# Kernel tuning notes

Measured on AMD Instinct MI355X. Metric: run time of the kernel, lower is better.

Reference implementation:

```python
import jax, jax.numpy as jnp
import numpy as np

NUM_BATCH, NUM_OBJ, NUM_DBOX, NUM_CLASSES = 64, 50, 8732, 2
JACCARD_THRESH = 0.5
NEGPOS_RATIO = 3
VARIANCE = (0.1, 0.2)


def setup_inputs() -> dict:
    key = jax.random.key(0)
    k1, k2, k3, k4, k5, k6 = jax.random.split(key, 6)
    loc_data = jax.random.normal(k1, (NUM_BATCH, NUM_DBOX, 4), dtype=jnp.float32)
    conf_data = jax.random.normal(k2, (NUM_BATCH, NUM_DBOX, NUM_CLASSES), dtype=jnp.float32)
    # default boxes in center-size form (cx, cy, w, h)
    cxcy = jax.random.uniform(k3, (NUM_DBOX, 2), minval=0.05, maxval=0.95)
    wh = jax.random.uniform(k4, (NUM_DBOX, 2), minval=0.05, maxval=0.4)
    dbox_list = jnp.concatenate([cxcy, wh], axis=1).astype(jnp.float32)
    # ground-truth boxes in point form [xmin,ymin,xmax,ymax] plus label (class 0 -> conf label 1)
    tc = jax.random.uniform(k5, (NUM_BATCH, NUM_OBJ, 2), minval=0.15, maxval=0.85)
    twh = jax.random.uniform(k6, (NUM_BATCH, NUM_OBJ, 2), minval=0.05, maxval=0.3)
    truths = jnp.concatenate([tc - twh / 2, tc + twh / 2], axis=-1)
    labels = jnp.zeros((NUM_BATCH, NUM_OBJ, 1), dtype=jnp.float32)
    targets = jnp.concatenate([truths, labels], axis=-1).astype(jnp.float32)
    return {"loc_data": loc_data, "conf_data": conf_data, "dbox_list": dbox_list, "targets": targets}


def point_form(boxes):
    # (cx,cy,w,h) -> (xmin,ymin,xmax,ymax)
    return jnp.concatenate([boxes[:, :2] - boxes[:, 2:] / 2, boxes[:, :2] + boxes[:, 2:] / 2], axis=1)


def jaccard(a, b):
    # a: [No,4], b: [Nd,4], both point form -> [No,Nd]
    lt = jnp.maximum(a[:, None, :2], b[None, :, :2])
    rb = jnp.minimum(a[:, None, 2:], b[None, :, 2:])
    wh = jnp.clip(rb - lt, 0.0)
    inter = wh[..., 0] * wh[..., 1]
    area_a = ((a[:, 2] - a[:, 0]) * (a[:, 3] - a[:, 1]))[:, None]
    area_b = ((b[:, 2] - b[:, 0]) * (b[:, 3] - b[:, 1]))[None, :]
    return inter / (area_a + area_b - inter)


def encode(matched, priors):
    # matched: [Nd,4] point form; priors: [Nd,4] center-size form
    g_cxcy = (matched[:, :2] + matched[:, 2:]) / 2 - priors[:, :2]
    g_cxcy = g_cxcy / (VARIANCE[0] * priors[:, 2:])
    g_wh = jnp.log((matched[:, 2:] - matched[:, :2]) / priors[:, 2:]) / VARIANCE[1]
    return jnp.concatenate([g_cxcy, g_wh], axis=1)


def match_one(truths, labels, dbox):
    # truths [No,4], labels [No], dbox [Nd,4] center-size
    overlaps = jaccard(truths, point_form(dbox))  # [No, Nd]
    best_prior_idx = jnp.argmax(overlaps, axis=1)          # [No]
    best_truth_overlap = jnp.max(overlaps, axis=0)          # [Nd]
    best_truth_idx = jnp.argmax(overlaps, axis=0)           # [Nd]
    best_truth_overlap = best_truth_overlap.at[best_prior_idx].set(2.0)
    best_truth_idx = best_truth_idx.at[best_prior_idx].set(jnp.arange(truths.shape[0]))
    matched = truths[best_truth_idx]                        # [Nd,4]
    conf = labels[best_truth_idx].astype(jnp.int32) + 1
    conf = jnp.where(best_truth_overlap < JACCARD_THRESH, 0, conf)
    loc = encode(matched, dbox)
    return loc, conf


def smooth_l1(x, t):
    d = jnp.abs(x - t)
    return jnp.where(d < 1.0, 0.5 * d * d, d - 0.5)


def cross_entropy(logits, labels):
    # logits [..., C], labels [...] int -> elementwise CE
    logp = jax.nn.log_softmax(logits, axis=-1)
    return -jnp.take_along_axis(logp, labels[..., None], axis=-1)[..., 0]


def reference(loc_data, conf_data, dbox_list, targets):
    num_batch, num_dbox, _ = loc_data.shape
    truths = targets[..., :-1]        # [B,No,4]
    labels = targets[..., -1]          # [B,No]
    loc_t, conf_t_label = jax.vmap(match_one, in_axes=(0, 0, None))(truths, labels, dbox_list)
    pos_mask = conf_t_label > 0        # [B,Nd]

    # localization loss: smooth L1 over positive priors, mean over selected elements
    l1 = smooth_l1(loc_data, loc_t)                               # [B,Nd,4]
    n_pos_elems = 4.0 * jnp.sum(pos_mask)
    loss_l = jnp.nan_to_num(jnp.sum(l1 * pos_mask[..., None]) / n_pos_elems)

    # per-prior confidence loss for hard-negative mining
    ce = cross_entropy(conf_data, conf_t_label)                   # [B,Nd]
    ce_mined = jnp.where(pos_mask, 0.0, ce)
    loss_idx = jnp.argsort(-ce_mined, axis=1)                     # descending sort
    idx_rank = jnp.argsort(loss_idx, axis=1)
    num_pos = jnp.sum(pos_mask, axis=1, keepdims=True)            # [B,1]
    num_neg = jnp.clip(num_pos * NEGPOS_RATIO, 20, num_dbox)
    neg_mask = idx_rank < num_neg                                 # [B,Nd]

    posf = pos_mask.astype(ce.dtype)
    negf = neg_mask.astype(ce.dtype)
    loss_c_pos = jnp.nan_to_num(jnp.sum(ce * posf) / jnp.sum(posf))
    loss_c_neg = jnp.nan_to_num(jnp.sum(ce * negf) / jnp.sum(negf))
    loss_c = loss_c_pos + loss_c_neg
    return jnp.stack([loss_l, loss_c, loss_c_pos, loss_c_neg])
```

## Files before the change

### kernel.cpp

```cpp
#include <hip/hip_runtime.h>

#define NB     64
#define NOBJ   50
#define ND     8732
#define PPT    3
#define BLK1   256
#define PRB    (BLK1*PPT)
#define NSPLIT ((ND + PRB - 1) / PRB)
#define NW1    (BLK1/64)
#define CHUNK  10
#define NCHUNK 5
#define BLK2   1024
#define NW2    (BLK2/64)
#define ITER2  ((ND + BLK2 - 1)/BLK2)

__device__ float              g_part[NB*5];
__device__ float              g_ov[(size_t)NB*ND];
__device__ unsigned short     g_idx[(size_t)NB*ND];
__device__ unsigned long long g_keys[(size_t)NB*NSPLIT*NW1*NOBJ];
__device__ int                g_done;

__global__ __launch_bounds__(BLK1) void k1_iou(const float* __restrict__ dbox,
                                               const float* __restrict__ targets) {
    __shared__ float s_tx1[NOBJ], s_ty1[NOBJ], s_tx2[NOBJ], s_ty2[NOBJ], s_area[NOBJ];
    const int blk  = blockIdx.x;
    const int b    = blk / NSPLIT;
    const int spl  = blk % NSPLIT;
    const int tid  = threadIdx.x;
    const int lane = tid & 63;
    const int wv   = tid >> 6;

    if (blk == 0 && tid == 0) g_done = 0;

    if (tid < NOBJ) {
        const float* t = targets + (b*NOBJ + tid)*5;
        float x1=t[0], y1=t[1], x2=t[2], y2=t[3];
        s_tx1[tid]=x1; s_ty1[tid]=y1; s_tx2[tid]=x2; s_ty2[tid]=y2;
        s_area[tid]=(x2-x1)*(y2-y1);
    }
    __syncthreads();

    const int d0  = spl * PRB;
    const int cnt = (ND - d0 < PRB) ? (ND - d0) : PRB;

    float px1[PPT], py1[PPT], px2[PPT], py2[PPT], pa[PPT];
    bool  vld[PPT];
    float bov[PPT]; int bj[PPT];
#pragma unroll
    for (int q = 0; q < PPT; ++q) {
        int dl = tid*PPT + q;
        vld[q] = dl < cnt;
        bov[q] = -1.0f; bj[q] = 0;
        px1[q]=py1[q]=px2[q]=py2[q]=0.f; pa[q]=0.f;
        if (vld[q]) {
            float4 p = reinterpret_cast<const float4*>(dbox)[d0 + dl];
            px1[q] = p.x - 0.5f*p.z; py1[q] = p.y - 0.5f*p.w;
            px2[q] = p.x + 0.5f*p.z; py2[q] = p.y + 0.5f*p.w;
            pa[q]  = p.z * p.w;
        }
    }

    unsigned long long* kout = g_keys + (((size_t)b*NSPLIT + spl)*NW1 + wv)*NOBJ;

    for (int c = 0; c < NCHUNK; ++c) {
        float ttx1[CHUNK],tty1[CHUNK],ttx2[CHUNK],tty2[CHUNK],tta[CHUNK];
#pragma unroll
        for (int jj=0;jj<CHUNK;++jj){ int j=c*CHUNK+jj;
            ttx1[jj]=s_tx1[j]; tty1[jj]=s_ty1[j]; ttx2[jj]=s_tx2[j]; tty2[jj]=s_ty2[j]; tta[jj]=s_area[j]; }
        float tb[CHUNK]; int td[CHUNK];
#pragma unroll
        for (int jj=0;jj<CHUNK;++jj){ tb[jj]=-1.0f; td[jj]=0; }

#pragma unroll
        for (int q=0;q<PPT;++q){
            if (!vld[q]) continue;
            const int d = d0 + tid*PPT + q;
#pragma unroll
            for (int jj=0;jj<CHUNK;++jj){
                float ltx=fmaxf(ttx1[jj],px1[q]), lty=fmaxf(tty1[jj],py1[q]);
                float rbx=fminf(ttx2[jj],px2[q]), rby=fminf(tty2[jj],py2[q]);
                float ww=fmaxf(rbx-ltx,0.f), hh=fmaxf(rby-lty,0.f);
                float inter=ww*hh;
                float iou=__fdividef(inter, tta[jj]+pa[q]-inter);
                if (iou>bov[q]){bov[q]=iou;bj[q]=c*CHUNK+jj;}
                if (iou>tb[jj]){tb[jj]=iou;td[jj]=d;}
            }
        }
#pragma unroll
        for (int jj=0;jj<CHUNK;++jj){
            float m = tb[jj];
#pragma unroll
            for (int off=32; off>=1; off>>=1)
                m = fmaxf(m, __shfl_xor(m, off, 64));
            unsigned long long msk = __ballot(tb[jj]==m);
            int lead = __builtin_ctzll(msk);
            int dwin = __shfl(td[jj], lead, 64);
            if (lane==0) {
                unsigned long long enc = (m>=0.f)
                  ? (((unsigned long long)__float_as_uint(m)<<32)
                     | (unsigned long long)(0xFFFFFFFFu - (unsigned)dwin))
                  : 0ull;
                kout[c*CHUNK+jj] = enc;
            }
        }
    }
#pragma unroll
    for (int q=0;q<PPT;++q){
        if (vld[q]) {
            int d = d0 + tid*PPT + q;
            g_ov [(size_t)b*ND + d] = bov[q];
            g_idx[(size_t)b*ND + d] = (unsigned short)bj[q];
        }
    }
}

__global__ __launch_bounds__(BLK2) void k2_loss(const float* __restrict__ loc_data,
                                                const float* __restrict__ conf_data,
                                                const float* __restrict__ dbox,
                                                const float* __restrict__ targets,
                                                float* __restrict__ out) {
    __shared__ float s_tx1[NOBJ],s_ty1[NOBJ],s_tx2[NOBJ],s_ty2[NOBJ],s_lab[NOBJ];
    __shared__ unsigned int   s_dj[NOBJ];
    __shared__ unsigned short s_ovr[ND];
    __shared__ float s_val[ND];
    __shared__ int   s_hist[NW2*256];
    __shared__ int   s_wtot[4];
    __shared__ float s_rf[NW2], s_rf2[NW2], s_rf3[NW2];
    __shared__ int   s_ri[NW2];
    __shared__ int   s_sel, s_krem, s_kk, s_last;

    const int b=blockIdx.x, tid=threadIdx.x, lane=tid&63, wv=tid>>6;

    for (int i=tid;i<ND;i+=BLK2) s_ovr[i]=0xFFFFu;
    if (tid<NOBJ){
        const float* t=targets+(b*NOBJ+tid)*5;
        s_tx1[tid]=t[0]; s_ty1[tid]=t[1]; s_tx2[tid]=t[2]; s_ty2[tid]=t[3]; s_lab[tid]=t[4];
        unsigned long long k0=0ull;
        const unsigned long long* kp = g_keys + (size_t)b*NSPLIT*NW1*NOBJ + tid;
#pragma unroll 1
        for (int s=0;s<NSPLIT*NW1;++s){ unsigned long long o=kp[(size_t)s*NOBJ]; if(o>k0)k0=o; }
        s_dj[tid]=0xFFFFFFFFu-(unsigned)(k0&0xFFFFFFFFull);
    }
    __syncthreads();
    if (tid<NOBJ){
        unsigned d=s_dj[tid]; bool win=true;
        for (int j2=tid+1;j2<NOBJ;++j2) if (s_dj[j2]==d){win=false;break;}
        if (win) s_ovr[d]=(unsigned short)tid;
    }
    __syncthreads();

    float ce[ITER2];
    float npos=0.f, sl1=0.f, scep=0.f;
#pragma unroll
    for (int it=0; it<ITER2; ++it){
        int d = tid + it*BLK2;
        float cm = 0.f;
        if (d < ND) {
            float ov = g_ov[(size_t)b*ND+d];
            int j    = (int)g_idx[(size_t)b*ND+d];
            unsigned short ovr = s_ovr[d];
            if (ovr != 0xFFFFu){ ov=2.0f; j=(int)ovr; }
            bool pos = !(ov < 0.5f);
            float2 cf = reinterpret_cast<const float2*>(conf_data)[(size_t)b*ND+d];
            float m = fmaxf(cf.x, cf.y);
            float lse = m + __logf(__expf(cf.x-m)+__expf(cf.y-m));
            int lab = pos ? ((int)s_lab[j] + 1) : 0;
            float ced = lse - (lab>=1 ? cf.y : cf.x);
            cm = pos ? 0.f : ced;
            if (pos){
                npos += 1.f; scep += ced;
                float4 p = reinterpret_cast<const float4*>(dbox)[d];
                float tx1=s_tx1[j],ty1=s_ty1[j],tx2=s_tx2[j],ty2=s_ty2[j];
                float g0=((tx1+tx2)*0.5f-p.x)/(0.1f*p.z);
                float g1=((ty1+ty2)*0.5f-p.y)/(0.1f*p.w);
                float g2=__logf((tx2-tx1)/p.z)*5.0f;
                float g3=__logf((ty2-ty1)/p.w)*5.0f;
                float4 ld = reinterpret_cast<const float4*>(loc_data)[(size_t)b*ND+d];
                float t0=fabsf(ld.x-g0),t1=fabsf(ld.y-g1),t2=fabsf(ld.z-g2),t3=fabsf(ld.w-g3);
                sl1 += (t0<1.f?0.5f*t0*t0:t0-0.5f) + (t1<1.f?0.5f*t1*t1:t1-0.5f)
                     + (t2<1.f?0.5f*t2*t2:t2-0.5f) + (t3<1.f?0.5f*t3*t3:t3-0.5f);
            }
            s_val[d]=cm;
        }
        ce[it]=cm;
    }
#pragma unroll
    for (int off=32;off>=1;off>>=1){
        npos+=__shfl_xor(npos,off,64);
        sl1 +=__shfl_xor(sl1 ,off,64);
        scep+=__shfl_xor(scep,off,64);
    }
    if (lane==0){s_rf[wv]=npos;s_rf2[wv]=sl1;s_rf3[wv]=scep;}
    __syncthreads();
    if (tid==0){
        float a=0,bb=0,cc=0;
        for(int w2=0;w2<NW2;++w2){a+=s_rf[w2];bb+=s_rf2[w2];cc+=s_rf3[w2];}
        int np=(int)a; int k=np*3; if(k<20)k=20; if(k>ND)k=ND;
        s_kk=k;
        g_part[b*5+0]=a; g_part[b*5+1]=bb; g_part[b*5+2]=cc; g_part[b*5+3]=(float)k;
    }
    __syncthreads();
    const int k = s_kk;

    unsigned prefix=0u, pmask=0u; int krem=k;
    for (int p=0;p<3;++p){
        const int shift = 24 - p*8;
        for (int i=tid;i<NW2*256;i+=BLK2) s_hist[i]=0;
        __syncthreads();
#pragma unroll
        for (int it=0;it<ITER2;++it){
            int d = tid + it*BLK2;
            if (d<ND){
                unsigned vb=__float_as_uint(ce[it]);
                if ((vb&pmask)==prefix)
                    atomicAdd(&s_hist[wv*256 + (int)((vb>>shift)&255u)],1);
            }
        }
        __syncthreads();
        int cnt=0, S=0, add=0;
        if (tid<256){
            for (int w2=0;w2<NW2;++w2) cnt+=s_hist[w2*256+tid];
            S=cnt;
#pragma unroll
            for (int off=1;off<64;off<<=1){
                int t=__shfl_down(S,off,64);
                if (lane+off<64) S+=t;
            }
            if (lane==0) s_wtot[wv]=S;
        }
        __syncthreads();
        if (tid<256){
            for (int w2=wv+1;w2<4;++w2) add+=s_wtot[w2];
            S+=add;
            int Snext=__shfl_down(S,1,64);
            if (lane==63) Snext=add;
            if (S>=krem && Snext<krem){ s_sel=tid; s_krem=krem-(S-cnt); }
        }
        __syncthreads();
        prefix |= ((unsigned)s_sel)<<shift;
        pmask  |= 255u<<shift;
        krem = s_krem;
    }
    const float T=__uint_as_float(prefix);

    int cgt=0; float sgt=0.f;
#pragma unroll
    for (int it=0;it<ITER2;++it){
        int d=tid+it*BLK2;
        if (d<ND){ float v=ce[it]; if (v>T){cgt++; sgt+=v;} }
    }
#pragma unroll
    for (int off=32;off>=1;off>>=1){ cgt+=__shfl_xor(cgt,off,64); sgt+=__shfl_xor(sgt,off,64); }
    if (lane==0){ s_ri[wv]=cgt; s_rf[wv]=sgt; }
    __syncthreads();
    if (tid==0){
        int cg=0; float sg=0.f;
        for(int w2=0;w2<NW2;++w2){cg+=s_ri[w2];sg+=s_rf[w2];}
        int need=k-cg;
        float stk=sg+(float)need*T;
        if (!(T>0.f) && need>0){
            int taken=0;
            for (int d=0; d<ND && taken<need; ++d){
                if (s_val[d]==0.f){
                    float ov=g_ov[(size_t)b*ND+d]; int j=(int)g_idx[(size_t)b*ND+d];
                    unsigned short ovr=s_ovr[d];
                    if (ovr!=0xFFFFu){ov=2.f;j=(int)ovr;}
                    bool pos=!(ov<0.5f);
                    float2 cf=reinterpret_cast<const float2*>(conf_data)[(size_t)b*ND+d];
                    float m=fmaxf(cf.x,cf.y);
                    float lse=m+__logf(__expf(cf.x-m)+__expf(cf.y-m));
                    int lab=pos?((int)s_lab[j]+1):0;
                    stk += lse-(lab>=1?cf.y:cf.x);
                    ++taken;
                }
            }
        }
        g_part[b*5+4]=stk;
    }

    if (tid==0){ __threadfence(); int old=atomicAdd(&g_done,1); s_last=(old==NB-1)?1:0; }
    __syncthreads();
    if (s_last && tid<NB){
        __threadfence();
        volatile float* gp = g_part;
        float np=gp[tid*5+0], sl=gp[tid*5+1], sc=gp[tid*5+2], kk=gp[tid*5+3], st=gp[tid*5+4];
#pragma unroll
        for (int off=32;off>=1;off>>=1){
            np+=__shfl_xor(np,off,64); sl+=__shfl_xor(sl,off,64);
            sc+=__shfl_xor(sc,off,64); kk+=__shfl_xor(kk,off,64); st+=__shfl_xor(st,off,64);
        }
        if (tid==0){
            float loss_l=(np>0.f)?sl/(4.f*np):0.f;
            float lcp=(np>0.f)?sc/np:0.f;
            float lcn=(kk>0.f)?st/kk:0.f;
            out[0]=loss_l; out[1]=lcp+lcn; out[2]=lcp; out[3]=lcn;
        }
    }
}

extern "C" void kernel_launch(void* const* d_in, const int* in_sizes, int n_in,
                              void* d_out, int out_size, void* d_ws, size_t ws_size,
                              hipStream_t stream) {
    const float* loc     = (const float*)d_in[0];
    const float* conf    = (const float*)d_in[1];
    const float* dboxp   = (const float*)d_in[2];
    const float* targets = (const float*)d_in[3];
    float* out = (float*)d_out;

    k1_iou<<<NB*NSPLIT, BLK1, 0, stream>>>(dboxp, targets);
    k2_loss<<<NB, BLK2, 0, stream>>>(loc, conf, dboxp, targets, out);
}
```

Before: 139.6 us.

## Move CE, positive losses and top-byte histogram into IoU kernel with forced-match fixups

The first kernel now computes per-prior cross-entropy, smooth-L1 and positive counts for the argmax match. It also writes a signed CE array and a per-block histogram of the top radix byte. The loss kernel then only applies corrections for the priors forced to match each object's best prior, adjusting sums and histogram entries. It reuses the precomputed histogram for the first radix pass and reads CE from shared memory. This moves the heavy per-prior work into the wide, many-block first kernel and removes one radix histogram pass from the 64-block kernel, at the cost of correction logic and extra global buffers.

Measured after the change: 123.5 us. -11.5%, faster.

```diff
diff --git a/kernel.cpp b/kernel.cpp
--- a/kernel.cpp
+++ b/kernel.cpp
@@ -6,294 +6,355 @@
 #define PPT    3
 #define BLK1   256
 #define PRB    (BLK1*PPT)
-#define NSPLIT ((ND + PRB - 1) / PRB)
+#define NSPLIT 12
 #define NW1    (BLK1/64)
+#define NPART  (NSPLIT*NW1)
 #define CHUNK  10
 #define NCHUNK 5
 #define BLK2   1024
 #define NW2    (BLK2/64)
-#define ITER2  ((ND + BLK2 - 1)/BLK2)
+#define ITER2  ((ND+BLK2-1)/BLK2)
+#define ND4    (ND/4)
 
 __device__ float              g_part[NB*5];
-__device__ float              g_ov[(size_t)NB*ND];
-__device__ unsigned short     g_idx[(size_t)NB*ND];
-__device__ unsigned long long g_keys[(size_t)NB*NSPLIT*NW1*NOBJ];
+__device__ float4             g_ce4[(size_t)NB*ND4];
+__device__ unsigned long long g_keys[(size_t)NB*NPART*NOBJ];
+__device__ int                g_hist[(size_t)NB*NSPLIT*256];
+__device__ float              g_bp[NB*NSPLIT*3];
 __device__ int                g_done;
 
-__global__ __launch_bounds__(BLK1) void k1_iou(const float* __restrict__ dbox,
-                                               const float* __restrict__ targets) {
-    __shared__ float s_tx1[NOBJ], s_ty1[NOBJ], s_tx2[NOBJ], s_ty2[NOBJ], s_area[NOBJ];
-    const int blk  = blockIdx.x;
-    const int b    = blk / NSPLIT;
-    const int spl  = blk % NSPLIT;
-    const int tid  = threadIdx.x;
-    const int lane = tid & 63;
-    const int wv   = tid >> 6;
-
-    if (blk == 0 && tid == 0) g_done = 0;
-
-    if (tid < NOBJ) {
-        const float* t = targets + (b*NOBJ + tid)*5;
-        float x1=t[0], y1=t[1], x2=t[2], y2=t[3];
-        s_tx1[tid]=x1; s_ty1[tid]=y1; s_tx2[tid]=x2; s_ty2[tid]=y2;
-        s_area[tid]=(x2-x1)*(y2-y1);
-    }
-    __syncthreads();
-
-    const int d0  = spl * PRB;
-    const int cnt = (ND - d0 < PRB) ? (ND - d0) : PRB;
-
-    float px1[PPT], py1[PPT], px2[PPT], py2[PPT], pa[PPT];
-    bool  vld[PPT];
-    float bov[PPT]; int bj[PPT];
-#pragma unroll
-    for (int q = 0; q < PPT; ++q) {
-        int dl = tid*PPT + q;
-        vld[q] = dl < cnt;
-        bov[q] = -1.0f; bj[q] = 0;
-        px1[q]=py1[q]=px2[q]=py2[q]=0.f; pa[q]=0.f;
-        if (vld[q]) {
-            float4 p = reinterpret_cast<const float4*>(dbox)[d0 + dl];
-            px1[q] = p.x - 0.5f*p.z; py1[q] = p.y - 0.5f*p.w;
-            px2[q] = p.x + 0.5f*p.z; py2[q] = p.y + 0.5f*p.w;
-            pa[q]  = p.z * p.w;
-        }
-    }
-
-    unsigned long long* kout = g_keys + (((size_t)b*NSPLIT + spl)*NW1 + wv)*NOBJ;
-
-    for (int c = 0; c < NCHUNK; ++c) {
-        float ttx1[CHUNK],tty1[CHUNK],ttx2[CHUNK],tty2[CHUNK],tta[CHUNK];
-#pragma unroll
-        for (int jj=0;jj<CHUNK;++jj){ int j=c*CHUNK+jj;
-            ttx1[jj]=s_tx1[j]; tty1[jj]=s_ty1[j]; ttx2[jj]=s_tx2[j]; tty2[jj]=s_ty2[j]; tta[jj]=s_area[j]; }
+__device__ __forceinline__ float iou_rn(float px1,float py1,float px2,float py2,float pa,
+                                        float tx1,float ty1,float tx2,float ty2,float ta){
+    float ltx=fmaxf(tx1,px1), lty=fmaxf(ty1,py1);
+    float rbx=fminf(tx2,px2), rby=fminf(ty2,py2);
+    float ww=fmaxf(__fsub_rn(rbx,ltx),0.f), hh=fmaxf(__fsub_rn(rby,lty),0.f);
+    float inter=__fmul_rn(ww,hh);
+    return __fdividef(inter, __fsub_rn(__fadd_rn(ta,pa),inter));
+}
+__device__ __forceinline__ float lse2(float x0,float x1){
+    float m=fmaxf(x0,x1);
+    return m+__logf(__expf(x0-m)+__expf(x1-m));
+}
+__device__ __forceinline__ float sl1_enc(float4 p,float tx1,float ty1,float tx2,float ty2,float4 ld){
+    float g0=((tx1+tx2)*0.5f-p.x)/(0.1f*p.z);
+    float g1=((ty1+ty2)*0.5f-p.y)/(0.1f*p.w);
+    float g2=__logf((tx2-tx1)/p.z)*5.0f;
+    float g3=__logf((ty2-ty1)/p.w)*5.0f;
+    float t0=fabsf(ld.x-g0),t1=fabsf(ld.y-g1),t2=fabsf(ld.z-g2),t3=fabsf(ld.w-g3);
+    return (t0<1.f?0.5f*t0*t0:t0-0.5f)+(t1<1.f?0.5f*t1*t1:t1-0.5f)
+          +(t2<1.f?0.5f*t2*t2:t2-0.5f)+(t3<1.f?0.5f*t3*t3:t3-0.5f);
+}
+
+__global__ __launch_bounds__(BLK1) void k1(const float* __restrict__ loc_data,
+                                           const float* __restrict__ conf_data,
+                                           const float* __restrict__ dbox,
+                                           const float* __restrict__ targets){
+    __shared__ float s_tx1[NOBJ],s_ty1[NOBJ],s_tx2[NOBJ],s_ty2[NOBJ],s_ta[NOBJ],s_lab[NOBJ];
+    __shared__ int   s_wh[NW1*256];
+    __shared__ float s_r1[NW1],s_r2[NW1],s_r3[NW1];
+    const int blk=blockIdx.x, b=blk/NSPLIT, spl=blk%NSPLIT;
+    const int tid=threadIdx.x, lane=tid&63, wv=tid>>6;
+    if (blk==0 && tid==0) g_done=0;
+    if (tid<NOBJ){
+        const float* t=targets+(b*NOBJ+tid)*5;
+        float x1=t[0],y1=t[1],x2=t[2],y2=t[3];
+        s_tx1[tid]=x1;s_ty1[tid]=y1;s_tx2[tid]=x2;s_ty2[tid]=y2;
+        s_ta[tid]=__fmul_rn(__fsub_rn(x2,x1),__fsub_rn(y2,y1));
+        s_lab[tid]=t[4];
+    }
+    for (int i=tid;i<NW1*256;i+=BLK1) s_wh[i]=0;
+    __syncthreads();
+
+    const int d0=spl*PRB;
+    const int cnt=(ND-d0<PRB)?(ND-d0):PRB;
+    float px1[PPT],py1[PPT],px2[PPT],py2[PPT],pa[PPT];
+    bool vld[PPT]; float bov[PPT]; int bj[PPT];
+#pragma unroll
+    for (int q=0;q<PPT;++q){
+        int dl=tid*PPT+q; vld[q]=dl<cnt; bov[q]=-1.f; bj[q]=0;
+        px1[q]=py1[q]=px2[q]=py2[q]=pa[q]=0.f;
+        if (vld[q]){
+            float4 p=reinterpret_cast<const float4*>(dbox)[d0+dl];
+            float hw=__fmul_rn(0.5f,p.z), hh=__fmul_rn(0.5f,p.w);
+            px1[q]=__fsub_rn(p.x,hw); py1[q]=__fsub_rn(p.y,hh);
+            px2[q]=__fadd_rn(p.x,hw); py2[q]=__fadd_rn(p.y,hh);
+            pa[q]=__fmul_rn(p.z,p.w);
+        }
+    }
+    unsigned long long* kout=g_keys+(((size_t)b*NSPLIT+spl)*NW1+wv)*NOBJ;
+
+    for (int c=0;c<NCHUNK;++c){
+        float tx1c[CHUNK],ty1c[CHUNK],tx2c[CHUNK],ty2c[CHUNK],tac[CHUNK];
+#pragma unroll
+        for (int jj=0;jj<CHUNK;++jj){int j=c*CHUNK+jj;
+            tx1c[jj]=s_tx1[j];ty1c[jj]=s_ty1[j];tx2c[jj]=s_tx2[j];ty2c[jj]=s_ty2[j];tac[jj]=s_ta[j];}
         float tb[CHUNK]; int td[CHUNK];
 #pragma unroll
-        for (int jj=0;jj<CHUNK;++jj){ tb[jj]=-1.0f; td[jj]=0; }
-
+        for (int jj=0;jj<CHUNK;++jj){tb[jj]=-1.f;td[jj]=0;}
 #pragma unroll
         for (int q=0;q<PPT;++q){
             if (!vld[q]) continue;
-            const int d = d0 + tid*PPT + q;
+            const int d=d0+tid*PPT+q;
 #pragma unroll
             for (int jj=0;jj<CHUNK;++jj){
-                float ltx=fmaxf(ttx1[jj],px1[q]), lty=fmaxf(tty1[jj],py1[q]);
-                float rbx=fminf(ttx2[jj],px2[q]), rby=fminf(tty2[jj],py2[q]);
-                float ww=fmaxf(rbx-ltx,0.f), hh=fmaxf(rby-lty,0.f);
-                float inter=ww*hh;
-                float iou=__fdividef(inter, tta[jj]+pa[q]-inter);
+                float iou=iou_rn(px1[q],py1[q],px2[q],py2[q],pa[q],
+                                 tx1c[jj],ty1c[jj],tx2c[jj],ty2c[jj],tac[jj]);
                 if (iou>bov[q]){bov[q]=iou;bj[q]=c*CHUNK+jj;}
                 if (iou>tb[jj]){tb[jj]=iou;td[jj]=d;}
             }
         }
 #pragma unroll
         for (int jj=0;jj<CHUNK;++jj){
-            float m = tb[jj];
-#pragma unroll
-            for (int off=32; off>=1; off>>=1)
-                m = fmaxf(m, __shfl_xor(m, off, 64));
-            unsigned long long msk = __ballot(tb[jj]==m);
-            int lead = __builtin_ctzll(msk);
-            int dwin = __shfl(td[jj], lead, 64);
-            if (lane==0) {
-                unsigned long long enc = (m>=0.f)
-                  ? (((unsigned long long)__float_as_uint(m)<<32)
-                     | (unsigned long long)(0xFFFFFFFFu - (unsigned)dwin))
-                  : 0ull;
-                kout[c*CHUNK+jj] = enc;
-            }
-        }
-    }
+            float m=tb[jj];
+#pragma unroll
+            for (int off=32;off>=1;off>>=1) m=fmaxf(m,__shfl_xor(m,off,64));
+            unsigned long long msk=__ballot(tb[jj]==m);
+            int lead=__builtin_ctzll(msk);
+            int dwin=__shfl(td[jj],lead,64);
+            if (lane==0){
+                unsigned long long enc=(m>=0.f)
+                    ?(((unsigned long long)__float_as_uint(m)<<32)
+                      |(unsigned long long)(0xFFFFFFFFu-(unsigned)dwin))
+                    :0ull;
+                kout[c*CHUNK+jj]=enc;
+            }
+        }
+    }
+
+    float* gce=(float*)g_ce4;
+    float np=0.f,sl=0.f,sc=0.f;
 #pragma unroll
     for (int q=0;q<PPT;++q){
-        if (vld[q]) {
-            int d = d0 + tid*PPT + q;
-            g_ov [(size_t)b*ND + d] = bov[q];
-            g_idx[(size_t)b*ND + d] = (unsigned short)bj[q];
-        }
-    }
-}
-
-__global__ __launch_bounds__(BLK2) void k2_loss(const float* __restrict__ loc_data,
-                                                const float* __restrict__ conf_data,
-                                                const float* __restrict__ dbox,
-                                                const float* __restrict__ targets,
-                                                float* __restrict__ out) {
-    __shared__ float s_tx1[NOBJ],s_ty1[NOBJ],s_tx2[NOBJ],s_ty2[NOBJ],s_lab[NOBJ];
-    __shared__ unsigned int   s_dj[NOBJ];
-    __shared__ unsigned short s_ovr[ND];
-    __shared__ float s_val[ND];
-    __shared__ int   s_hist[NW2*256];
-    __shared__ int   s_wtot[4];
-    __shared__ float s_rf[NW2], s_rf2[NW2], s_rf3[NW2];
-    __shared__ int   s_ri[NW2];
-    __shared__ int   s_sel, s_krem, s_kk, s_last;
+        if (!vld[q]) continue;
+        const int d=d0+tid*PPT+q;
+        float2 cf=reinterpret_cast<const float2*>(conf_data)[(size_t)b*ND+d];
+        float l=lse2(cf.x,cf.y);
+        bool pos=!(bov[q]<0.5f);
+        int jb=bj[q];
+        int lab=pos?((int)s_lab[jb]+1):0;
+        float cev=l-(lab>=1?cf.y:cf.x);
+        float raw=pos?-cev:cev;
+        gce[(size_t)b*ND+d]=raw;
+        atomicAdd(&s_wh[wv*256+(int)(__float_as_uint(fmaxf(raw,0.f))>>24)],1);
+        if (pos){
+            np+=1.f; sc+=cev;
+            float4 p=reinterpret_cast<const float4*>(dbox)[d];
+            float4 ldv=reinterpret_cast<const float4*>(loc_data)[(size_t)b*ND+d];
+            sl+=sl1_enc(p,s_tx1[jb],s_ty1[jb],s_tx2[jb],s_ty2[jb],ldv);
+        }
+    }
+#pragma unroll
+    for (int off=32;off>=1;off>>=1){
+        np+=__shfl_xor(np,off,64); sl+=__shfl_xor(sl,off,64); sc+=__shfl_xor(sc,off,64);
+    }
+    if (lane==0){s_r1[wv]=np;s_r2[wv]=sl;s_r3[wv]=sc;}
+    __syncthreads();
+    if (tid==0){
+        float a=0.f,bb2=0.f,cc=0.f;
+        for (int w=0;w<NW1;++w){a+=s_r1[w];bb2+=s_r2[w];cc+=s_r3[w];}
+        g_bp[(b*NSPLIT+spl)*3+0]=a;
+        g_bp[(b*NSPLIT+spl)*3+1]=bb2;
+        g_bp[(b*NSPLIT+spl)*3+2]=cc;
+    }
+    {
+        int s=0;
+        for (int w=0;w<NW1;++w) s+=s_wh[w*256+tid];
+        g_hist[(size_t)(b*NSPLIT+spl)*256+tid]=s;
+    }
+}
+
+__global__ __launch_bounds__(BLK2) void k2(const float* __restrict__ loc_data,
+                                           const float* __restrict__ conf_data,
+                                           const float* __restrict__ dbox,
+                                           const float* __restrict__ targets,
+                                           float* __restrict__ out){
+    __shared__ float4 s_ce4[ND4];
+    __shared__ unsigned long long s_km[NOBJ*16];
+    __shared__ unsigned int s_dj[NOBJ];
+    __shared__ float s_tx1[NOBJ],s_ty1[NOBJ],s_tx2[NOBJ],s_ty2[NOBJ],s_ta[NOBJ],s_lab[NOBJ];
+    __shared__ int   s_hist[256];
+    __shared__ int   s_wh[NW2*256];
+    __shared__ float s_bpl[NSPLIT*3];
+    __shared__ float s_rf[NW2]; __shared__ int s_ri[NW2];
+    __shared__ int   s_wt[4];
+    __shared__ float s_dnp,s_dsl,s_dsc;
+    __shared__ int   s_sel,s_krem,s_kk,s_last;
+    float* s_ce=(float*)s_ce4;
 
     const int b=blockIdx.x, tid=threadIdx.x, lane=tid&63, wv=tid>>6;
 
-    for (int i=tid;i<ND;i+=BLK2) s_ovr[i]=0xFFFFu;
     if (tid<NOBJ){
         const float* t=targets+(b*NOBJ+tid)*5;
-        s_tx1[tid]=t[0]; s_ty1[tid]=t[1]; s_tx2[tid]=t[2]; s_ty2[tid]=t[3]; s_lab[tid]=t[4];
-        unsigned long long k0=0ull;
-        const unsigned long long* kp = g_keys + (size_t)b*NSPLIT*NW1*NOBJ + tid;
-#pragma unroll 1
-        for (int s=0;s<NSPLIT*NW1;++s){ unsigned long long o=kp[(size_t)s*NOBJ]; if(o>k0)k0=o; }
-        s_dj[tid]=0xFFFFFFFFu-(unsigned)(k0&0xFFFFFFFFull);
-    }
-    __syncthreads();
+        float x1=t[0],y1=t[1],x2=t[2],y2=t[3];
+        s_tx1[tid]=x1;s_ty1[tid]=y1;s_tx2[tid]=x2;s_ty2[tid]=y2;
+        s_ta[tid]=__fmul_rn(__fsub_rn(x2,x1),__fsub_rn(y2,y1));
+        s_lab[tid]=t[4];
+    }
+    if (tid<NOBJ*16){
+        int j=tid>>4, s=tid&15;
+        const unsigned long long* kp=g_keys+(size_t)b*NPART*NOBJ;
+        unsigned long long m=kp[(size_t)s*NOBJ+j];
+        unsigned long long o=kp[(size_t)(s+16)*NOBJ+j]; if(o>m)m=o;
+        o=kp[(size_t)(s+32)*NOBJ+j]; if(o>m)m=o;
+        s_km[tid]=m;
+    }
+    for (int i=tid;i<ND4;i+=BLK2) s_ce4[i]=g_ce4[(size_t)b*ND4+i];
+    if (tid<256){
+        int s=0;
+        for (int sp=0;sp<NSPLIT;++sp) s+=g_hist[(size_t)(b*NSPLIT+sp)*256+tid];
+        s_hist[tid]=s;
+    }
+    if (tid<NSPLIT*3) s_bpl[tid]=g_bp[b*NSPLIT*3+tid];
+    __syncthreads();
+    if (tid<NOBJ){
+        unsigned long long m=s_km[tid*16];
+        for (int s=1;s<16;++s){unsigned long long o=s_km[tid*16+s]; if(o>m)m=o;}
+        s_dj[tid]=0xFFFFFFFFu-(unsigned)(m&0xFFFFFFFFull);
+    }
+    __syncthreads();
+
+    float dnp=0.f,dsl=0.f,dsc=0.f;
     if (tid<NOBJ){
         unsigned d=s_dj[tid]; bool win=true;
         for (int j2=tid+1;j2<NOBJ;++j2) if (s_dj[j2]==d){win=false;break;}
-        if (win) s_ovr[d]=(unsigned short)tid;
-    }
-    __syncthreads();
-
-    float ce[ITER2];
-    float npos=0.f, sl1=0.f, scep=0.f;
-#pragma unroll
-    for (int it=0; it<ITER2; ++it){
-        int d = tid + it*BLK2;
-        float cm = 0.f;
-        if (d < ND) {
-            float ov = g_ov[(size_t)b*ND+d];
-            int j    = (int)g_idx[(size_t)b*ND+d];
-            unsigned short ovr = s_ovr[d];
-            if (ovr != 0xFFFFu){ ov=2.0f; j=(int)ovr; }
-            bool pos = !(ov < 0.5f);
-            float2 cf = reinterpret_cast<const float2*>(conf_data)[(size_t)b*ND+d];
-            float m = fmaxf(cf.x, cf.y);
-            float lse = m + __logf(__expf(cf.x-m)+__expf(cf.y-m));
-            int lab = pos ? ((int)s_lab[j] + 1) : 0;
-            float ced = lse - (lab>=1 ? cf.y : cf.x);
-            cm = pos ? 0.f : ced;
-            if (pos){
-                npos += 1.f; scep += ced;
-                float4 p = reinterpret_cast<const float4*>(dbox)[d];
-                float tx1=s_tx1[j],ty1=s_ty1[j],tx2=s_tx2[j],ty2=s_ty2[j];
-                float g0=((tx1+tx2)*0.5f-p.x)/(0.1f*p.z);
-                float g1=((ty1+ty2)*0.5f-p.y)/(0.1f*p.w);
-                float g2=__logf((tx2-tx1)/p.z)*5.0f;
-                float g3=__logf((ty2-ty1)/p.w)*5.0f;
-                float4 ld = reinterpret_cast<const float4*>(loc_data)[(size_t)b*ND+d];
-                float t0=fabsf(ld.x-g0),t1=fabsf(ld.y-g1),t2=fabsf(ld.z-g2),t3=fabsf(ld.w-g3);
-                sl1 += (t0<1.f?0.5f*t0*t0:t0-0.5f) + (t1<1.f?0.5f*t1*t1:t1-0.5f)
-                     + (t2<1.f?0.5f*t2*t2:t2-0.5f) + (t3<1.f?0.5f*t3*t3:t3-0.5f);
-            }
-            s_val[d]=cm;
-        }
-        ce[it]=cm;
-    }
-#pragma unroll
-    for (int off=32;off>=1;off>>=1){
-        npos+=__shfl_xor(npos,off,64);
-        sl1 +=__shfl_xor(sl1 ,off,64);
-        scep+=__shfl_xor(scep,off,64);
-    }
-    if (lane==0){s_rf[wv]=npos;s_rf2[wv]=sl1;s_rf3[wv]=scep;}
+        if (win){
+            float4 p=reinterpret_cast<const float4*>(dbox)[d];
+            float hw=__fmul_rn(0.5f,p.z), hh2=__fmul_rn(0.5f,p.w);
+            float ppx1=__fsub_rn(p.x,hw),ppy1=__fsub_rn(p.y,hh2);
+            float ppx2=__fadd_rn(p.x,hw),ppy2=__fadd_rn(p.y,hh2);
+            float ppa=__fmul_rn(p.z,p.w);
+            float bov=-1.f; int jb=0;
+            for (int j=0;j<NOBJ;++j){
+                float iou=iou_rn(ppx1,ppy1,ppx2,ppy2,ppa,
+                                 s_tx1[j],s_ty1[j],s_tx2[j],s_ty2[j],s_ta[j]);
+                if (iou>bov){bov=iou;jb=j;}
+            }
+            bool oldpos=!(bov<0.5f);
+            float2 cf=reinterpret_cast<const float2*>(conf_data)[(size_t)b*ND+d];
+            float l=lse2(cf.x,cf.y);
+            float4 ldv=reinterpret_cast<const float4*>(loc_data)[(size_t)b*ND+d];
+            int labN=(int)s_lab[tid]+1;
+            float ceN=l-(labN>=1?cf.y:cf.x);
+            dsc+=ceN; dsl+=sl1_enc(p,s_tx1[tid],s_ty1[tid],s_tx2[tid],s_ty2[tid],ldv);
+            if (oldpos){
+                int labO=(int)s_lab[jb]+1;
+                float ceO=l-(labO>=1?cf.y:cf.x);
+                dsc-=ceO; dsl-=sl1_enc(p,s_tx1[jb],s_ty1[jb],s_tx2[jb],s_ty2[jb],ldv);
+            } else dnp+=1.f;
+            float oldraw=s_ce[d];
+            atomicAdd(&s_hist[(int)(__float_as_uint(fmaxf(oldraw,0.f))>>24)],-1);
+            atomicAdd(&s_hist[0],1);
+            s_ce[d]=-ceN;
+        }
+    }
+    if (wv==0){
+#pragma unroll
+        for (int off=32;off>=1;off>>=1){
+            dnp+=__shfl_xor(dnp,off,64); dsl+=__shfl_xor(dsl,off,64); dsc+=__shfl_xor(dsc,off,64);
+        }
+        if (lane==0){s_dnp=dnp;s_dsl=dsl;s_dsc=dsc;}
+    }
     __syncthreads();
     if (tid==0){
-        float a=0,bb=0,cc=0;
-        for(int w2=0;w2<NW2;++w2){a+=s_rf[w2];bb+=s_rf2[w2];cc+=s_rf3[w2];}
-        int np=(int)a; int k=np*3; if(k<20)k=20; if(k>ND)k=ND;
+        float np=s_dnp, sl=s_dsl, sc=s_dsc;
+        for (int i=0;i<NSPLIT;++i){np+=s_bpl[i*3];sl+=s_bpl[i*3+1];sc+=s_bpl[i*3+2];}
+        int npi=(int)np; int k=npi*3; if(k<20)k=20; if(k>ND)k=ND;
         s_kk=k;
-        g_part[b*5+0]=a; g_part[b*5+1]=bb; g_part[b*5+2]=cc; g_part[b*5+3]=(float)k;
-    }
-    __syncthreads();
-    const int k = s_kk;
-
-    unsigned prefix=0u, pmask=0u; int krem=k;
+        g_part[b*5+0]=np; g_part[b*5+1]=sl; g_part[b*5+2]=sc; g_part[b*5+3]=(float)k;
+    }
+    __syncthreads();
+    const int k=s_kk;
+
+    unsigned prefix=0u,pmask=0u; int krem=k;
     for (int p=0;p<3;++p){
-        const int shift = 24 - p*8;
-        for (int i=tid;i<NW2*256;i+=BLK2) s_hist[i]=0;
-        __syncthreads();
-#pragma unroll
-        for (int it=0;it<ITER2;++it){
-            int d = tid + it*BLK2;
-            if (d<ND){
-                unsigned vb=__float_as_uint(ce[it]);
-                if ((vb&pmask)==prefix)
-                    atomicAdd(&s_hist[wv*256 + (int)((vb>>shift)&255u)],1);
-            }
-        }
-        __syncthreads();
-        int cnt=0, S=0, add=0;
+        const int shift=24-p*8;
+        int cnt=0;
+        if (p==0){
+            if (tid<256) cnt=s_hist[tid];
+        } else {
+            for (int i=tid;i<NW2*256;i+=BLK2) s_wh[i]=0;
+            __syncthreads();
+            for (int it=0;it<ITER2;++it){
+                int d=tid+it*BLK2;
+                if (d<ND){
+                    unsigned vb=__float_as_uint(fmaxf(s_ce[d],0.f));
+                    if ((vb&pmask)==prefix)
+                        atomicAdd(&s_wh[wv*256+(int)((vb>>shift)&255u)],1);
+                }
+            }
+            __syncthreads();
+            if (tid<256){
+                for (int w=0;w<NW2;++w) cnt+=s_wh[w*256+tid];
+            }
+        }
+        int S=cnt,add=0;
         if (tid<256){
-            for (int w2=0;w2<NW2;++w2) cnt+=s_hist[w2*256+tid];
-            S=cnt;
 #pragma unroll
             for (int off=1;off<64;off<<=1){
                 int t=__shfl_down(S,off,64);
                 if (lane+off<64) S+=t;
             }
-            if (lane==0) s_wtot[wv]=S;
+            if (lane==0) s_wt[wv]=S;
         }
         __syncthreads();
         if (tid<256){
-            for (int w2=wv+1;w2<4;++w2) add+=s_wtot[w2];
+            for (int w=wv+1;w<4;++w) add+=s_wt[w];
             S+=add;
             int Snext=__shfl_down(S,1,64);
             if (lane==63) Snext=add;
-            if (S>=krem && Snext<krem){ s_sel=tid; s_krem=krem-(S-cnt); }
+            if (S>=krem && Snext<krem){s_sel=tid;s_krem=krem-(S-cnt);}
         }
         __syncthreads();
-        prefix |= ((unsigned)s_sel)<<shift;
-        pmask  |= 255u<<shift;
-        krem = s_krem;
+        prefix|=((unsigned)s_sel)<<shift;
+        pmask|=255u<<shift;
+        krem=s_krem;
+        __syncthreads();
     }
     const float T=__uint_as_float(prefix);
 
     int cgt=0; float sgt=0.f;
-#pragma unroll
     for (int it=0;it<ITER2;++it){
         int d=tid+it*BLK2;
-        if (d<ND){ float v=ce[it]; if (v>T){cgt++; sgt+=v;} }
-    }
-#pragma unroll
-    for (int off=32;off>=1;off>>=1){ cgt+=__shfl_xor(cgt,off,64); sgt+=__shfl_xor(sgt,off,64); }
-    if (lane==0){ s_ri[wv]=cgt; s_rf[wv]=sgt; }
+        if (d<ND){
+            float v=fmaxf(s_ce[d],0.f);
+            if (v>T){cgt++;sgt+=v;}
+        }
+    }
+#pragma unroll
+    for (int off=32;off>=1;off>>=1){cgt+=__shfl_xor(cgt,off,64);sgt+=__shfl_xor(sgt,off,64);}
+    if (lane==0){s_ri[wv]=cgt;s_rf[wv]=sgt;}
     __syncthreads();
     if (tid==0){
         int cg=0; float sg=0.f;
-        for(int w2=0;w2<NW2;++w2){cg+=s_ri[w2];sg+=s_rf[w2];}
+        for (int w=0;w<NW2;++w){cg+=s_ri[w];sg+=s_rf[w];}
         int need=k-cg;
         float stk=sg+(float)need*T;
-        if (!(T>0.f) && need>0){
+        if (!(T>0.f)&&need>0){
             int taken=0;
-            for (int d=0; d<ND && taken<need; ++d){
-                if (s_val[d]==0.f){
-                    float ov=g_ov[(size_t)b*ND+d]; int j=(int)g_idx[(size_t)b*ND+d];
-                    unsigned short ovr=s_ovr[d];
-                    if (ovr!=0xFFFFu){ov=2.f;j=(int)ovr;}
-                    bool pos=!(ov<0.5f);
-                    float2 cf=reinterpret_cast<const float2*>(conf_data)[(size_t)b*ND+d];
-                    float m=fmaxf(cf.x,cf.y);
-                    float lse=m+__logf(__expf(cf.x-m)+__expf(cf.y-m));
-                    int lab=pos?((int)s_lab[j]+1):0;
-                    stk += lse-(lab>=1?cf.y:cf.x);
-                    ++taken;
-                }
+            for (int d=0;d<ND&&taken<need;++d){
+                float r=s_ce[d];
+                if (!(r>0.f)){stk+=fabsf(r);++taken;}
             }
         }
         g_part[b*5+4]=stk;
     }
 
-    if (tid==0){ __threadfence(); int old=atomicAdd(&g_done,1); s_last=(old==NB-1)?1:0; }
-    __syncthreads();
-    if (s_last && tid<NB){
+    if (tid==0){__threadfence(); int old=atomicAdd(&g_done,1); s_last=(old==NB-1)?1:0;}
+    __syncthreads();
+    if (s_last&&tid<NB){
         __threadfence();
-        volatile float* gp = g_part;
-        float np=gp[tid*5+0], sl=gp[tid*5+1], sc=gp[tid*5+2], kk=gp[tid*5+3], st=gp[tid*5+4];
+        volatile float* gp=g_part;
+        float np=gp[tid*5+0],sl=gp[tid*5+1],sc=gp[tid*5+2],kk=gp[tid*5+3],st=gp[tid*5+4];
 #pragma unroll
         for (int off=32;off>=1;off>>=1){
-            np+=__shfl_xor(np,off,64); sl+=__shfl_xor(sl,off,64);
-            sc+=__shfl_xor(sc,off,64); kk+=__shfl_xor(kk,off,64); st+=__shfl_xor(st,off,64);
+            np+=__shfl_xor(np,off,64);sl+=__shfl_xor(sl,off,64);
+            sc+=__shfl_xor(sc,off,64);kk+=__shfl_xor(kk,off,64);st+=__shfl_xor(st,off,64);
         }
         if (tid==0){
             float loss_l=(np>0.f)?sl/(4.f*np):0.f;
             float lcp=(np>0.f)?sc/np:0.f;
             float lcn=(kk>0.f)?st/kk:0.f;
-            out[0]=loss_l; out[1]=lcp+lcn; out[2]=lcp; out[3]=lcn;
+            out[0]=loss_l;out[1]=lcp+lcn;out[2]=lcp;out[3]=lcn;
         }
     }
 }
@@ -307,6 +368,6 @@
     const float* targets = (const float*)d_in[3];
     float* out = (float*)d_out;
 
-    k1_iou<<<NB*NSPLIT, BLK1, 0, stream>>>(dboxp, targets);
-    k2_loss<<<NB, BLK2, 0, stream>>>(loc, conf, dboxp, targets, out);
-}
+    k1<<<NB*NSPLIT, BLK1, 0, stream>>>(loc, conf, dboxp, targets);
+    k2<<<NB, BLK2, 0, stream>>>(loc, conf, dboxp, targets, out);
+}
```
